# Kernel optimization log

Hardware: AMD Instinct MI355X
Metric: run time of the kernel (lower is better)

## Reference

```python
import jax, jax.numpy as jnp
import numpy as np

# Fixed reactor dimensions and grey-box constants (from hyb_greybox_pars / xuyscales)
NX, NU, NY, NP = 3, 1, 2, 4
NZ = NP * (NY + NU)          # 12
F, V, DELTA = 0.1, 1.0, 1.0
CAMEAN, CBMEAN = 1.0, 0.5    # yscale mean
CASTD, CBSTD = 0.5, 0.3      # yscale std
CAFMEAN, CAFSTD = 2.0, 0.5   # uscale


def _fnn(x, layers):
    """Feed-forward NN: tanh hidden layers, linear output layer."""
    for W, b in layers[:-1]:
        x = jnp.tanh(x @ W + b)
    W, b = layers[-1]
    return x @ W + b


def setup_inputs() -> dict:
    key = jax.random.key(0)
    ks = jax.random.split(key, 16)
    B, T = 2048, 1024
    d = {
        "useq": jax.random.normal(ks[0], (B, T, NU), jnp.float32),
        "x0": 0.1 * jax.random.normal(ks[1], (B, NX + NZ), jnp.float32),
    }
    s1 = 1.0 / np.sqrt(1.0)
    s16 = 1.0 / np.sqrt(16.0)
    s12 = 1.0 / np.sqrt(12.0)
    s32 = 1.0 / np.sqrt(32.0)
    for i, name in enumerate(["r1", "r2", "r3"]):
        d[name + "_W0"] = s1 * jax.random.normal(ks[2 + 2 * i], (1, 16), jnp.float32)
        d[name + "_b0"] = jnp.zeros((16,), jnp.float32)
        d[name + "_W1"] = s16 * jax.random.normal(ks[3 + 2 * i], (16, 1), jnp.float32)
        d[name + "_b1"] = jnp.zeros((1,), jnp.float32)
    d["estC_W0"] = s12 * jax.random.normal(ks[10], (12, 32), jnp.float32)
    d["estC_b0"] = jnp.zeros((32,), jnp.float32)
    d["estC_W1"] = s32 * jax.random.normal(ks[11], (32, 1), jnp.float32)
    d["estC_b1"] = jnp.zeros((1,), jnp.float32)
    return d


def reference(useq, x0,
              r1_W0, r1_b0, r1_W1, r1_b1,
              r2_W0, r2_b0, r2_W1, r2_b1,
              r3_W0, r3_b0, r3_W1, r3_b1,
              estC_W0, estC_b0, estC_W1, estC_b1):
    r1L = [(r1_W0, r1_b0), (r1_W1, r1_b1)]
    r2L = [(r2_W0, r2_b0), (r2_W1, r2_b1)]
    r3L = [(r3_W0, r3_b0), (r3_W1, r3_b1)]
    estCL = [(estC_W0, estC_b0), (estC_W1, estC_b1)]

    def fxu(x, u):
        Ca, Cb, Cc = x[:, 0:1], x[:, 1:2], x[:, 2:3]
        Caf = u[:, 0:1]
        r1 = _fnn(Ca, r1L) * CASTD
        r2 = _fnn(Cb, r2L) * CBSTD
        r3 = _fnn(Cc, r3L) * CBSTD
        Ca = Ca * CASTD + CAMEAN
        Cb = Cb * CBSTD + CBMEAN
        Cc = Cc * CBSTD + CBMEAN
        Caf = Caf * CAFSTD + CAFMEAN
        dCa = F * (Caf - Ca) / V - r1
        dCb = -F * Cb / V + r1 - 3.0 * r2 + r3
        dCc = -F * Cc / V + r2 - r3
        return jnp.concatenate([dCa / CASTD, dCb / CBSTD, dCc / CBSTD], axis=-1)

    def step(xz, u):
        x, z = xz[:, :NX], xz[:, NX:]
        ypseq, upseq = z[:, :NP * NY], z[:, NP * NY:]
        k1 = fxu(x, u)
        k2 = fxu(x + DELTA * (k1 / 2.0), u)
        k3 = fxu(x + DELTA * (k2 / 2.0), u)
        k4 = fxu(x + DELTA * k3, u)
        xplus = x + (DELTA / 6.0) * (k1 + 2.0 * k2 + 2.0 * k3 + k4)
        zplus = jnp.concatenate([ypseq[:, NY:], x[:, :NY], upseq[:, NU:], u], axis=-1)
        CcNN = _fnn(z, estCL)
        y = jnp.concatenate([x, CcNN], axis=-1)   # [B, Ny + 2*numUnmeasGb] = [B, 4]
        return jnp.concatenate([xplus, zplus], axis=-1), y

    u_t = jnp.swapaxes(useq, 0, 1)                # [T, B, Nu]
    _, ys = jax.lax.scan(step, x0, u_t)           # ys: [T, B, 4]
    return jnp.swapaxes(ys, 0, 1)                 # [B, T, 4]
```

## Files before the change

kernel.cpp:

```cpp
#include <hip/hip_runtime.h>

#define TT 1024
#define BB 2048
#define K1 8
#define L2E2 2.8853900817779268f

template <int CTRL>
__device__ __forceinline__ float dpp_add(float x) {
  int y = __builtin_amdgcn_update_dpp(0, __float_as_int(x), CTRL, 0xF, 0xF, true);
  return x + __int_as_float(y);
}
__device__ __forceinline__ float sum16(float x) {
  x = dpp_add<0xB1>(x);
  x = dpp_add<0x4E>(x);
  x = dpp_add<0x141>(x);
  x = dpp_add<0x140>(x);
  return x;
}
__device__ __forceinline__ float rdlane(float x, int l) {
  return __int_as_float(__builtin_amdgcn_readlane(__float_as_int(x), l));
}

__global__ __launch_bounds__(256) void phase1_kernel(
    const float* __restrict__ useq, const float* __restrict__ x0,
    const float* __restrict__ r1W0, const float* __restrict__ r1b0,
    const float* __restrict__ r1W1, const float* __restrict__ r1b1,
    const float* __restrict__ r2W0, const float* __restrict__ r2b0,
    const float* __restrict__ r2W1, const float* __restrict__ r2b1,
    const float* __restrict__ r3W0, const float* __restrict__ r3b0,
    const float* __restrict__ r3W1, const float* __restrict__ r3b1,
    float* __restrict__ out) {
  const int lane = threadIdx.x & 63;
  const int row = lane >> 4;
  const int j = lane & 15;
  const int e =
      __builtin_amdgcn_readfirstlane(blockIdx.x * 4 + (threadIdx.x >> 6));

  const float* W0p = (row == 0) ? r1W0 : (row == 1) ? r2W0 : r3W0;
  const float* b0p = (row == 0) ? r1b0 : (row == 1) ? r2b0 : r3b0;
  const float* W1p = (row == 0) ? r1W1 : (row == 1) ? r2W1 : r3W1;

  const float w0s = W0p[j] * L2E2;
  const float b0s = b0p[j] * L2E2;
  const float wn = -2.0f * W1p[j];

  float C1 = r1b1[0], C2 = r2b1[0], C3 = r3b1[0];
  for (int q = 0; q < 16; ++q) {
    C1 += r1W1[q];
    C2 += r2W1[q];
    C3 += r3W1[q];
  }
  const float caC = 0.2f - C1;
  const float cbC = -1.0f / 6.0f + (5.0f / 3.0f) * C1 - 3.0f * C2 + C3;
  const float ccC = -1.0f / 6.0f + C2 - C3;

  const float cstBase = (row == 0) ? caC : (row == 1) ? cbC : ccC;
  const float uco = (row == 0) ? 0.1f : 0.0f;
  const float a1 = (row == 0) ? -1.0f : (row == 1) ? (5.0f / 3.0f) : 0.0f;
  const float a2 = (row == 1) ? -3.0f : (row == 2) ? 1.0f : 0.0f;
  const float a3 = (row == 1) ? 1.0f : (row == 2) ? -1.0f : 0.0f;

  float S = x0[e * 15 + ((row < 3) ? row : 2)];

  const float* up = useq + e * TT;
  float* op = out + (size_t)e * TT * 4;

#define STAGE(SS, KK)                                                     \
  {                                                                       \
    float rv = __builtin_amdgcn_rcpf(                                     \
        __builtin_amdgcn_exp2f(fmaf(w0s, (SS), b0s)) + 1.0f);             \
    float q = sum16(wn * rv);                                             \
    float P1 = rdlane(q, 0);                                              \
    float P2 = rdlane(q, 16);                                             \
    float P3 = rdlane(q, 32);                                             \
    float t_ = fmaf(-0.1f, (SS), cstS);                                   \
    t_ = fmaf(a1, P1, t_);                                                \
    t_ = fmaf(a2, P2, t_);                                                \
    KK = fmaf(a3, P3, t_);                                                \
  }

#define STEP(UQ, SC_)                                                     \
  {                                                                       \
    const float cstS = fmaf(uco, (UQ), cstBase);                          \
    SC_ = S;                                                              \
    float k1, k2, k3, k4;                                                 \
    STAGE(S, k1)                                                          \
    float s2 = fmaf(0.5f, k1, S);                                         \
    STAGE(s2, k2)                                                         \
    float s3 = fmaf(0.5f, k2, S);                                         \
    STAGE(s3, k3)                                                         \
    float s4 = S + k3;                                                    \
    STAGE(s4, k4)                                                         \
    S = fmaf(1.0f / 6.0f, fmaf(2.0f, k2 + k3, k1) + k4, S);               \
  }

  float uc0, uc1, uc2, uc3, uc4, uc5, uc6, uc7;
  {
    float4 a = *(const float4*)(up);
    float4 b = *(const float4*)(up + 4);
    uc0 = a.x; uc1 = a.y; uc2 = a.z; uc3 = a.w;
    uc4 = b.x; uc5 = b.y; uc6 = b.z; uc7 = b.w;
  }

  for (int t0 = 0; t0 < TT; t0 += K1) {
    const int tn = (t0 + K1 <= TT - K1) ? (t0 + K1) : (TT - K1);
    const float4 na = *(const float4*)(up + tn);
    const float4 nb = *(const float4*)(up + tn + 4);

    float sc0, sc1, sc2, sc3, sc4, sc5, sc6, sc7;
    STEP(uc0, sc0)
    STEP(uc1, sc1)
    STEP(uc2, sc2)
    STEP(uc3, sc3)
    STEP(uc4, sc4)
    STEP(uc5, sc5)
    STEP(uc6, sc6)
    STEP(uc7, sc7)

    if (j == 0 && row < 3) {
      float* p = op + t0 * 4 + row;
      p[0] = sc0;  p[4] = sc1;  p[8] = sc2;  p[12] = sc3;
      p[16] = sc4; p[20] = sc5; p[24] = sc6; p[28] = sc7;
    }

    uc0 = na.x; uc1 = na.y; uc2 = na.z; uc3 = na.w;
    uc4 = nb.x; uc5 = nb.y; uc6 = nb.z; uc7 = nb.w;
  }
#undef STEP
#undef STAGE
}

__global__ __launch_bounds__(256) void phase2_kernel(
    const float* __restrict__ useq, const float* __restrict__ x0,
    const float* __restrict__ W0, const float* __restrict__ b0,
    const float* __restrict__ W1, const float* __restrict__ b1p,
    float* __restrict__ out) {
  __shared__ float4 wrow[32][4];
  for (int idx = threadIdx.x; idx < 512; idx += 256) {
    const int h = idx >> 4, r = idx & 15;
    float v = 0.0f;
    if (r < 12) v = W0[r * 32 + h] * L2E2;
    else if (r == 12) v = b0[h] * L2E2;
    else if (r == 13) v = -2.0f * W1[h];
    ((float*)&wrow[h][0])[r] = v;
  }
  __syncthreads();

  float base = b1p[0];
#pragma unroll
  for (int h = 0; h < 32; ++h) base += W1[h];

  const int b = blockIdx.x;
  const float* xrow = x0 + b * 15;

  float z[4][12];
#pragma unroll
  for (int k = 0; k < 4; ++k) {
    const int t = k * 256 + (int)threadIdx.x;
    const int g = (b << 10) + t;
    if (t >= 4) {
      const float* px = out + (size_t)g * 4;
#pragma unroll
      for (int i = 0; i < 4; ++i) {
        z[k][2 * i] = px[(i - 4) * 4 + 0];
        z[k][2 * i + 1] = px[(i - 4) * 4 + 1];
      }
      const float* pu = useq + g;
#pragma unroll
      for (int i = 0; i < 4; ++i) z[k][8 + i] = pu[i - 4];
    } else {
#pragma unroll
      for (int i = 0; i < 4; ++i) {
        const int s4 = t - 4 + i;
        const float* py = (s4 >= 0) ? (out + ((size_t)(b << 10) + s4) * 4)
                                    : (xrow + 3 + 2 * (i + t));
        z[k][2 * i] = py[0];
        z[k][2 * i + 1] = py[1];
        const float* pu = (s4 >= 0) ? (useq + (b << 10) + s4)
                                    : (xrow + 11 + i + t);
        z[k][8 + i] = pu[0];
      }
    }
  }

  float ov0 = base, ov1 = base, ov2 = base, ov3 = base;
#pragma unroll
  for (int h = 0; h < 32; ++h) {
    const float4 wa = wrow[h][0];
    const float4 wb = wrow[h][1];
    const float4 wc = wrow[h][2];
    const float4 wd = wrow[h][3];
#define ACC(OV, ZZ)                                                       \
  {                                                                       \
    float a = wd.x;                                                       \
    a = fmaf(ZZ[0], wa.x, a);  a = fmaf(ZZ[1], wa.y, a);                  \
    a = fmaf(ZZ[2], wa.z, a);  a = fmaf(ZZ[3], wa.w, a);                  \
    a = fmaf(ZZ[4], wb.x, a);  a = fmaf(ZZ[5], wb.y, a);                  \
    a = fmaf(ZZ[6], wb.z, a);  a = fmaf(ZZ[7], wb.w, a);                  \
    a = fmaf(ZZ[8], wc.x, a);  a = fmaf(ZZ[9], wc.y, a);                  \
    a = fmaf(ZZ[10], wc.z, a); a = fmaf(ZZ[11], wc.w, a);                 \
    const float r = __builtin_amdgcn_rcpf(__builtin_amdgcn_exp2f(a) + 1.0f); \
    OV = fmaf(wd.y, r, OV);                                               \
  }
    ACC(ov0, z[0])
    ACC(ov1, z[1])
    ACC(ov2, z[2])
    ACC(ov3, z[3])
#undef ACC
  }

  const size_t gb = (size_t)(b << 10) + threadIdx.x;
  out[(gb + 0) * 4 + 3] = ov0;
  out[(gb + 256) * 4 + 3] = ov1;
  out[(gb + 512) * 4 + 3] = ov2;
  out[(gb + 768) * 4 + 3] = ov3;
}

extern "C" void kernel_launch(void* const* d_in, const int* in_sizes, int n_in,
                              void* d_out, int out_size, void* d_ws,
                              size_t ws_size, hipStream_t stream) {
  const float* useq = (const float*)d_in[0];
  const float* x0 = (const float*)d_in[1];
  float* out = (float*)d_out;

  phase1_kernel<<<BB / 4, 256, 0, stream>>>(
      useq, x0,
      (const float*)d_in[2], (const float*)d_in[3], (const float*)d_in[4],
      (const float*)d_in[5], (const float*)d_in[6], (const float*)d_in[7],
      (const float*)d_in[8], (const float*)d_in[9], (const float*)d_in[10],
      (const float*)d_in[11], (const float*)d_in[12], (const float*)d_in[13],
      out);

  phase2_kernel<<<BB, 256, 0, stream>>>(
      useq, x0, (const float*)d_in[14], (const float*)d_in[15],
      (const float*)d_in[16], (const float*)d_in[17], out);
}
```

Measured before the change: 476.3 us.

## Fuse estC network into recurrence kernel, drop second phase kernel

Computes the estC MLP output inside the sequential phase1 loop, using lane n&31 for hidden units and a 32-lane DPP+swizzle reduction. The z history is kept in registers and shifted each step. This removes the phase2 launch and its re-reads of out and useq. In exchange, every time step on the serial critical path gets extra ALU, exp/rcp and cross-lane work.

```diff
diff --git a/kernel.cpp b/kernel.cpp
--- a/kernel.cpp
+++ b/kernel.cpp
@@ -16,6 +16,11 @@
   x = dpp_add<0x141>(x);
   x = dpp_add<0x140>(x);
   return x;
+}
+__device__ __forceinline__ float sum32(float x) {
+  x = sum16(x);
+  int y = __builtin_amdgcn_ds_swizzle(__float_as_int(x), 0x401F);
+  return x + __int_as_float(y);
 }
 __device__ __forceinline__ float rdlane(float x, int l) {
   return __int_as_float(__builtin_amdgcn_readlane(__float_as_int(x), l));
@@ -29,6 +34,8 @@
     const float* __restrict__ r2W1, const float* __restrict__ r2b1,
     const float* __restrict__ r3W0, const float* __restrict__ r3b0,
     const float* __restrict__ r3W1, const float* __restrict__ r3b1,
+    const float* __restrict__ eW0, const float* __restrict__ eb0p,
+    const float* __restrict__ eW1, const float* __restrict__ eb1p,
     float* __restrict__ out) {
   const int lane = threadIdx.x & 63;
   const int row = lane >> 4;
@@ -61,6 +68,31 @@
   const float a3 = (row == 1) ? 1.0f : (row == 2) ? -1.0f : 0.0f;
 
   float S = x0[e * 15 + ((row < 3) ? row : 2)];
+
+  const int n = lane & 31;
+  float ew0_, ew1_, ew2_, ew3_, ew4_, ew5_, ew6_, ew7_, ew8_, ew9_, ew10_,
+      ew11_;
+  ew0_ = eW0[0 * 32 + n] * L2E2;
+  ew1_ = eW0[1 * 32 + n] * L2E2;
+  ew2_ = eW0[2 * 32 + n] * L2E2;
+  ew3_ = eW0[3 * 32 + n] * L2E2;
+  ew4_ = eW0[4 * 32 + n] * L2E2;
+  ew5_ = eW0[5 * 32 + n] * L2E2;
+  ew6_ = eW0[6 * 32 + n] * L2E2;
+  ew7_ = eW0[7 * 32 + n] * L2E2;
+  ew8_ = eW0[8 * 32 + n] * L2E2;
+  ew9_ = eW0[9 * 32 + n] * L2E2;
+  ew10_ = eW0[10 * 32 + n] * L2E2;
+  ew11_ = eW0[11 * 32 + n] * L2E2;
+  const float eb0 = eb0p[n] * L2E2;
+  const float ew1n = -2.0f * eW1[n];
+  float ebase = eb1p[0];
+  for (int q = 0; q < 32; ++q) ebase += eW1[q];
+
+  const float* zp = x0 + e * 15 + 3;
+  float hy0 = zp[0], hy1 = zp[1], hy2 = zp[2], hy3 = zp[3];
+  float hy4 = zp[4], hy5 = zp[5], hy6 = zp[6], hy7 = zp[7];
+  float hu0 = zp[8], hu1 = zp[9], hu2 = zp[10], hu3 = zp[11];
 
   const float* up = useq + e * TT;
   float* op = out + (size_t)e * TT * 4;
@@ -79,10 +111,31 @@
     KK = fmaf(a3, P3, t_);                                                \
   }
 
+#define ESTC(Y3_)                                                         \
+  {                                                                       \
+    float a_ = eb0;                                                       \
+    a_ = fmaf(hy0, ew0_, a_);  a_ = fmaf(hy1, ew1_, a_);                  \
+    a_ = fmaf(hy2, ew2_, a_);  a_ = fmaf(hy3, ew3_, a_);                  \
+    a_ = fmaf(hy4, ew4_, a_);  a_ = fmaf(hy5, ew5_, a_);                  \
+    a_ = fmaf(hy6, ew6_, a_);  a_ = fmaf(hy7, ew7_, a_);                  \
+    a_ = fmaf(hu0, ew8_, a_);  a_ = fmaf(hu1, ew9_, a_);                  \
+    a_ = fmaf(hu2, ew10_, a_); a_ = fmaf(hu3, ew11_, a_);                 \
+    float er_ = __builtin_amdgcn_rcpf(                                    \
+        __builtin_amdgcn_exp2f(a_) + 1.0f);                               \
+    Y3_ = ebase + sum32(ew1n * er_);                                      \
+  }
+
 #define STEP(UQ, SC_)                                                     \
   {                                                                       \
+    float y3_;                                                            \
+    ESTC(y3_)                                                             \
     const float cstS = fmaf(uco, (UQ), cstBase);                          \
-    SC_ = S;                                                              \
+    SC_ = (row == 3) ? y3_ : S;                                           \
+    const float yA_ = rdlane(S, 0);                                       \
+    const float yB_ = rdlane(S, 16);                                      \
+    hy0 = hy2; hy1 = hy3; hy2 = hy4; hy3 = hy5;                           \
+    hy4 = hy6; hy5 = hy7; hy6 = yA_; hy7 = yB_;                           \
+    hu0 = hu1; hu1 = hu2; hu2 = hu3; hu3 = (UQ);                          \
     float k1, k2, k3, k4;                                                 \
     STAGE(S, k1)                                                          \
     float s2 = fmaf(0.5f, k1, S);                                         \
@@ -117,7 +170,7 @@
     STEP(uc6, sc6)
     STEP(uc7, sc7)
 
-    if (j == 0 && row < 3) {
+    if (j == 0) {
       float* p = op + t0 * 4 + row;
       p[0] = sc0;  p[4] = sc1;  p[8] = sc2;  p[12] = sc3;
       p[16] = sc4; p[20] = sc5; p[24] = sc6; p[28] = sc7;
@@ -127,93 +180,8 @@
     uc4 = nb.x; uc5 = nb.y; uc6 = nb.z; uc7 = nb.w;
   }
 #undef STEP
+#undef ESTC
 #undef STAGE
-}
-
-__global__ __launch_bounds__(256) void phase2_kernel(
-    const float* __restrict__ useq, const float* __restrict__ x0,
-    const float* __restrict__ W0, const float* __restrict__ b0,
-    const float* __restrict__ W1, const float* __restrict__ b1p,
-    float* __restrict__ out) {
-  __shared__ float4 wrow[32][4];
-  for (int idx = threadIdx.x; idx < 512; idx += 256) {
-    const int h = idx >> 4, r = idx & 15;
-    float v = 0.0f;
-    if (r < 12) v = W0[r * 32 + h] * L2E2;
-    else if (r == 12) v = b0[h] * L2E2;
-    else if (r == 13) v = -2.0f * W1[h];
-    ((float*)&wrow[h][0])[r] = v;
-  }
-  __syncthreads();
-
-  float base = b1p[0];
-#pragma unroll
-  for (int h = 0; h < 32; ++h) base += W1[h];
-
-  const int b = blockIdx.x;
-  const float* xrow = x0 + b * 15;
-
-  float z[4][12];
-#pragma unroll
-  for (int k = 0; k < 4; ++k) {
-    const int t = k * 256 + (int)threadIdx.x;
-    const int g = (b << 10) + t;
-    if (t >= 4) {
-      const float* px = out + (size_t)g * 4;
-#pragma unroll
-      for (int i = 0; i < 4; ++i) {
-        z[k][2 * i] = px[(i - 4) * 4 + 0];
-        z[k][2 * i + 1] = px[(i - 4) * 4 + 1];
-      }
-      const float* pu = useq + g;
-#pragma unroll
-      for (int i = 0; i < 4; ++i) z[k][8 + i] = pu[i - 4];
-    } else {
-#pragma unroll
-      for (int i = 0; i < 4; ++i) {
-        const int s4 = t - 4 + i;
-        const float* py = (s4 >= 0) ? (out + ((size_t)(b << 10) + s4) * 4)
-                                    : (xrow + 3 + 2 * (i + t));
-        z[k][2 * i] = py[0];
-        z[k][2 * i + 1] = py[1];
-        const float* pu = (s4 >= 0) ? (useq + (b << 10) + s4)
-                                    : (xrow + 11 + i + t);
-        z[k][8 + i] = pu[0];
-      }
-    }
-  }
-
-  float ov0 = base, ov1 = base, ov2 = base, ov3 = base;
-#pragma unroll
-  for (int h = 0; h < 32; ++h) {
-    const float4 wa = wrow[h][0];
-    const float4 wb = wrow[h][1];
-    const float4 wc = wrow[h][2];
-    const float4 wd = wrow[h][3];
-#define ACC(OV, ZZ)                                                       \
-  {                                                                       \
-    float a = wd.x;                                                       \
-    a = fmaf(ZZ[0], wa.x, a);  a = fmaf(ZZ[1], wa.y, a);                  \
-    a = fmaf(ZZ[2], wa.z, a);  a = fmaf(ZZ[3], wa.w, a);                  \
-    a = fmaf(ZZ[4], wb.x, a);  a = fmaf(ZZ[5], wb.y, a);                  \
-    a = fmaf(ZZ[6], wb.z, a);  a = fmaf(ZZ[7], wb.w, a);                  \
-    a = fmaf(ZZ[8], wc.x, a);  a = fmaf(ZZ[9], wc.y, a);                  \
-    a = fmaf(ZZ[10], wc.z, a); a = fmaf(ZZ[11], wc.w, a);                 \
-    const float r = __builtin_amdgcn_rcpf(__builtin_amdgcn_exp2f(a) + 1.0f); \
-    OV = fmaf(wd.y, r, OV);                                               \
-  }
-    ACC(ov0, z[0])
-    ACC(ov1, z[1])
-    ACC(ov2, z[2])
-    ACC(ov3, z[3])
-#undef ACC
-  }
-
-  const size_t gb = (size_t)(b << 10) + threadIdx.x;
-  out[(gb + 0) * 4 + 3] = ov0;
-  out[(gb + 256) * 4 + 3] = ov1;
-  out[(gb + 512) * 4 + 3] = ov2;
-  out[(gb + 768) * 4 + 3] = ov3;
 }
 
 extern "C" void kernel_launch(void* const* d_in, const int* in_sizes, int n_in,
@@ -229,9 +197,6 @@
       (const float*)d_in[5], (const float*)d_in[6], (const float*)d_in[7],
       (const float*)d_in[8], (const float*)d_in[9], (const float*)d_in[10],
       (const float*)d_in[11], (const float*)d_in[12], (const float*)d_in[13],
-      out);
-
-  phase2_kernel<<<BB, 256, 0, stream>>>(
-      useq, x0, (const float*)d_in[14], (const float*)d_in[15],
-      (const float*)d_in[16], (const float*)d_in[17], out);
-}
+      (const float*)d_in[14], (const float*)d_in[15], (const float*)d_in[16],
+      (const float*)d_in[17], out);
+}
```

Result: slower. 520.3 us (+9.2%).
